# Performance work log

Hardware: AMD Instinct MI355X
Metric: run time of the kernel (lower is better)

Reference implementation:

```python
import jax, jax.numpy as jnp
import numpy as np
from jax import lax

T = 600000   # raw waveform samples (divisible by first_stride=5)
CIN = 256    # channels
L = T // 5   # output frames


def _leaky(x):
    return jnp.where(x >= 0, x, 0.3 * x)


def _quantize(x, scale, offset):
    # div + round + int8 cast + float cast; clip emulates the int8 range
    return jnp.clip(jnp.round(x / scale - offset), -128.0, 127.0)


def _dequantize(x, scale, offset):
    return (x + offset) * scale


def _conv1d(x, w, stride=1, dilation=1, groups=1):
    # x: [B, W, C]; w: [K, Cin/groups, Cout]; VALID padding (buffers provide causal pad)
    return lax.conv_general_dilated(
        x, w, window_strides=(stride,), padding='VALID',
        rhs_dilation=(dilation,), dimension_numbers=('NWC', 'WIO', 'NWC'),
        feature_group_count=groups)


def _res_block(x, w_dw, b_dw, w_pw, b_pw, w_lc, b_lc, dilation, qp=None, dqp=None):
    C = x.shape[-1]
    h = _conv1d(x, w_dw, dilation=dilation, groups=C) + b_dw   # depthwise (3,1)
    h = _conv1d(h, w_pw) + b_pw                                # pointwise 1x1
    if qp is not None:
        h = _quantize(h, *qp)
    h = _leaky(h)
    h = _conv1d(h, w_lc) + b_lc                                # last 1x1
    if dqp is not None:
        h = _dequantize(h, *dqp)
    return h


def setup_inputs() -> dict:
    key = jax.random.key(0)
    ks = jax.random.split(key, 32)
    rn = lambda k, s, sc=0.05: jax.random.normal(k, s, dtype=jnp.float32) * sc
    inp = {
        'x': rn(ks[0], (1, T, 1, 1), 1.0),
        'first_buffer': jnp.zeros((1, 5, 1, 1), jnp.float32),
        'res1_buffer': jnp.zeros((1, 2, 1, CIN), jnp.float32),
        'res2_buffer': jnp.zeros((1, 6, 1, CIN), jnp.float32),
        'res3_buffer': jnp.zeros((1, 18, 1, CIN), jnp.float32),
        'w_first': rn(ks[1], (10, 1, CIN)),
        'b_first': rn(ks[2], (CIN,)),
    }
    i = 3
    for r in (1, 2, 3):
        inp['w_dw%d' % r] = rn(ks[i], (3, 1, CIN)); i += 1
        inp['b_dw%d' % r] = rn(ks[i], (CIN,)); i += 1
        inp['w_pw%d' % r] = rn(ks[i], (1, CIN, CIN)); i += 1
        inp['b_pw%d' % r] = rn(ks[i], (CIN,)); i += 1
        inp['w_lc%d' % r] = rn(ks[i], (1, CIN, CIN)); i += 1
        inp['b_lc%d' % r] = rn(ks[i], (CIN,)); i += 1
    return inp


def reference(x, first_buffer, res1_buffer, res2_buffer, res3_buffer,
              w_first, b_first,
              w_dw1, b_dw1, w_pw1, b_pw1, w_lc1, b_lc1,
              w_dw2, b_dw2, w_pw2, b_pw2, w_lc2, b_lc2,
              w_dw3, b_dw3, w_pw3, b_pw3, w_lc3, b_lc3):
    sq = lambda a: a[:, :, 0, :]  # [B,T,1,C] -> [B,T,C]; spatial W dim is always 1
    xs = sq(jnp.concatenate([first_buffer, x], axis=1))        # causal pad: [1,T+5,1]
    res_in = _conv1d(xs, w_first, stride=5) + b_first          # [1,L,CIN]
    ci = _leaky(res_in)
    ci = jnp.concatenate([sq(res1_buffer), ci], axis=1)        # pad 2 for dil-1 k3
    ro = _res_block(ci, w_dw1, b_dw1, w_pw1, b_pw1, w_lc1, b_lc1, dilation=1,
                    qp=(17.62967872619629, -67.0), dqp=(6.528060436248779, -16.0))
    res_in = res_in + ro
    res_in = _quantize(res_in, 12.716455459594727, -23.0)
    ci = _dequantize(_leaky(res_in), 5.548006534576416, 47.0)
    ci = jnp.concatenate([sq(res2_buffer), ci], axis=1)        # pad 6 for dil-3 k3
    ci = _quantize(ci, 5.548006534576416, 47.0)
    ro = _res_block(ci, w_dw2, b_dw2, w_pw2, b_pw2, w_lc2, b_lc2, dilation=3)
    res_in = ro + res_in
    ci = _dequantize(_leaky(res_in), 4.458680152893066, 38.0)
    ci = jnp.concatenate([sq(res3_buffer), ci], axis=1)        # pad 18 for dil-9 k3
    ci = _quantize(ci, 4.458680152893066, 38.0)
    ro = _res_block(ci, w_dw3, b_dw3, w_pw3, b_pw3, w_lc3, b_lc3, dilation=9)
    res_in = ro + res_in
    out = _dequantize(_leaky(res_in), 3.698859930038452, 34.0)
    return out[:, :, None, :]  # [1, L, 1, CIN]
```

## Files before the change

### kernel.cpp

```cpp
#include <hip/hip_runtime.h>


#define CIN   256
#define LOUT  120000
#define TIN   600000
#define FB    128
#define NBLK  ((LOUT + FB - 1) / FB)

typedef float fx4 __attribute__((ext_vector_type(4)));
typedef short bx8 __attribute__((ext_vector_type(8)));

#define BF_OFF   0
#define CI1_OFF  32768
#define R2R_OFF  50176
#define C3R_OFF  60056
#define XW_OFF   73056
#define LUT_OFF  73760
#define LDS_SZ   74016

__device__ __forceinline__ float lrelu(float v){ return v >= 0.0f ? v : 0.3f*v; }
__device__ __forceinline__ float clip8(float v){ return fminf(fmaxf(v, -128.0f), 127.0f); }
__device__ __forceinline__ unsigned short f2bf(float f){
  unsigned u = __builtin_bit_cast(unsigned, f);
  return (unsigned short)((u + 0x7FFFu + ((u >> 16) & 1u)) >> 16);
}
__device__ __forceinline__ float bf2f(unsigned short h){
  unsigned u = ((unsigned)h) << 16;
  return __builtin_bit_cast(float, u);
}
__device__ __forceinline__ unsigned cvtpk(float a, float b){
  unsigned r;
  asm("v_cvt_pk_bf16_f32 %0, %1, %2" : "=v"(r) : "v"(a), "v"(b));
  return r;
}

__device__ __forceinline__ void gemm_mfma(const char* __restrict__ Aw,
                                          const char* __restrict__ Bf,
                                          int lofs, fx4 acc[2][2])
{
#pragma unroll 1
  for (int kk = 0; kk < 8; ++kk) {
    bx8 Bh0 = *(const bx8*)(Bf + kk*4096 +        lofs);
    bx8 Bl0 = *(const bx8*)(Bf + kk*4096 + 1024 + lofs);
    bx8 Bh1 = *(const bx8*)(Bf + kk*4096 + 2048 + lofs);
    bx8 Bl1 = *(const bx8*)(Bf + kk*4096 + 3072 + lofs);
#pragma unroll
    for (int mt = 0; mt < 2; ++mt) {
      bx8 Ah = *(const bx8*)(Aw + (mt*8 + kk)*2048 +        lofs);
      bx8 Al = *(const bx8*)(Aw + (mt*8 + kk)*2048 + 1024 + lofs);
      acc[mt][0] = __builtin_amdgcn_mfma_f32_16x16x32_bf16(Ah, Bh0, acc[mt][0], 0, 0, 0);
      acc[mt][0] = __builtin_amdgcn_mfma_f32_16x16x32_bf16(Al, Bh0, acc[mt][0], 0, 0, 0);
      acc[mt][0] = __builtin_amdgcn_mfma_f32_16x16x32_bf16(Ah, Bl0, acc[mt][0], 0, 0, 0);
      acc[mt][1] = __builtin_amdgcn_mfma_f32_16x16x32_bf16(Ah, Bh1, acc[mt][1], 0, 0, 0);
      acc[mt][1] = __builtin_amdgcn_mfma_f32_16x16x32_bf16(Al, Bh1, acc[mt][1], 0, 0, 0);
      acc[mt][1] = __builtin_amdgcn_mfma_f32_16x16x32_bf16(Ah, Bl1, acc[mt][1], 0, 0, 0);
    }
  }
}

__global__ void pack_w(const float* __restrict__ w0, const float* __restrict__ w1,
                       const float* __restrict__ w2, const float* __restrict__ w3,
                       const float* __restrict__ w4, const float* __restrict__ w5,
                       char* __restrict__ Apk)
{
  const int l = blockIdx.x*256 + threadIdx.x;
  const int lane = l & 63, kk = (l >> 6) & 7, wm = (l >> 9) & 15, mat = l >> 13;
  const float* W = mat==0?w0 : mat==1?w1 : mat==2?w2 : mat==3?w3 : mat==4?w4 : w5;
  const int oc = wm*16 + (lane & 15);
  const int k0 = kk*32 + (lane >> 4)*8;
  unsigned short h[8], lo[8];
#pragma unroll
  for (int j = 0; j < 8; ++j) {
    const float v = W[(k0 + j)*CIN + oc];
    h[j]  = f2bf(v);
    lo[j] = f2bf(v - bf2f(h[j]));
  }
  char* base = Apk + mat*262144 + (wm*8 + kk)*2048 + lane*16;
  *(ushort4*)(base)        = make_ushort4(h[0],  h[1],  h[2],  h[3]);
  *(ushort4*)(base + 8)    = make_ushort4(h[4],  h[5],  h[6],  h[7]);
  *(ushort4*)(base + 1024) = make_ushort4(lo[0], lo[1], lo[2], lo[3]);
  *(ushort4*)(base + 1032) = make_ushort4(lo[4], lo[5], lo[6], lo[7]);
}

__launch_bounds__(512, 4)
__global__ void enc_kernel(const float* __restrict__ x,
                           const char* __restrict__ Apk,
                           const float* __restrict__ w_first, const float* __restrict__ b_first,
                           const float* __restrict__ w_dw1, const float* __restrict__ b_dw1,
                           const float* __restrict__ b_pw1, const float* __restrict__ b_lc1,
                           const float* __restrict__ w_dw2, const float* __restrict__ b_dw2,
                           const float* __restrict__ b_pw2, const float* __restrict__ b_lc2,
                           const float* __restrict__ w_dw3, const float* __restrict__ b_dw3,
                           const float* __restrict__ b_pw3, const float* __restrict__ b_lc3,
                           float* __restrict__ out)
{
  __shared__ __align__(16) char lds[LDS_SZ];
  const int tid  = threadIdx.x;
  const int lane = tid & 63;
  const int wv   = tid >> 6;
  const int qq   = lane >> 4;
  const int nn   = lane & 15;
  const int lofs = lane * 16;
  const int ch   = tid & 255;
  const int hf   = tid >> 8;
  const int t0   = blockIdx.x * FB;
  const fx4 fz = {0.0f, 0.0f, 0.0f, 0.0f};
  const char* Awv = Apk + wv*32768;

  volatile int vz = 0;

  if (tid < 256) {
    const float r  = (float)(tid - 128);
    const float dq = (lrelu(r) + 47.0f) * 5.548006534576416f;
    const float c  = clip8(rintf(dq / 5.548006534576416f - 47.0f));
    *(signed char*)&lds[LUT_OFF + tid] = (signed char)(int)c;
  }

  const int wofs_c = (ch >> 5)*4096 + (((ch & 31) >> 3)*16)*16 + (ch & 7)*2;

  int c0m[2];
#pragma unroll
  for (int mt = 0; mt < 2; ++mt) c0m[mt] = wv*32 + mt*16 + qq*4;

  fx4 acc[2][2];

  for (int pass = 0; pass < 5; ++pass) {
    const int pt0 = t0 - 32 + pass*32;
    const int xbase = 5*pt0 - 15;

    const int z = vz;
    const float* wfq  = w_first + z; const float* bfq  = b_first + z;
    const float* wd1q = w_dw1 + z;   const float* bd1q = b_dw1 + z;
    const float* wd2q = w_dw2 + z;   const float* bd2q = b_dw2 + z;
    const float* wd3q = w_dw3 + z;   const float* bd3q = b_dw3 + z;
    const float* bp1q = b_pw1 + z;   const float* bl1q = b_lc1 + z;
    const float* bp2q = b_pw2 + z;   const float* bl2q = b_lc2 + z;
    const float* bp3q = b_pw3 + z;   const float* bl3q = b_lc3 + z;

    float resf[2][2][4];

    __syncthreads();
    if (tid < 176) {
      const int gx = xbase + tid;
      *(float*)&lds[XW_OFF + tid*4] = (gx >= 0 && gx < TIN) ? x[gx] : 0.0f;
    }
    __syncthreads();

    {
      float wf[10];
#pragma unroll
      for (int k = 0; k < 10; ++k) wf[k] = wfq[k*CIN + ch];
      const float bfv = bfq[ch];
      const int j0 = hf * 17;
      for (int j = j0; j < j0 + 17; ++j) {
        const int t = pt0 + j - 2;
        float a = 0.0f;
#pragma unroll
        for (int k = 0; k < 10; ++k)
          a = fmaf(*(const float*)&lds[XW_OFF + (5*j + k)*4], wf[k], a);
        const float ci = (t < 0) ? 0.0f : lrelu(a + bfv);
        *(unsigned short*)&lds[CI1_OFF + (ch*34 + j)*2] = (unsigned short)cvtpk(ci, ci);
      }
    }
    __syncthreads();

    {
      const float d10 = wd1q[ch], d11 = wd1q[CIN+ch], d12 = wd1q[2*CIN+ch];
      const float bd1 = bd1q[ch];
      for (int s = 0; s < 16; ++s) {
        const int jr = hf*16 + ((s + tid) & 15);
        const float c2 = bf2f(*(const unsigned short*)&lds[CI1_OFF + (ch*34 + jr    )*2]);
        const float c1 = bf2f(*(const unsigned short*)&lds[CI1_OFF + (ch*34 + jr + 1)*2]);
        const float c0 = bf2f(*(const unsigned short*)&lds[CI1_OFF + (ch*34 + jr + 2)*2]);
        const float v = fmaf(d10, c2, fmaf(d11, c1, fmaf(d12, c0, bd1)));
        const int ab = wofs_c + ((jr >> 4)*2048) + ((jr & 15)*16);
        const unsigned hp = cvtpk(v, v);
        const float hb = __builtin_bit_cast(float, hp << 16);
        const unsigned lp = cvtpk(v - hb, v - hb);
        *(unsigned short*)&lds[BF_OFF + ab]        = (unsigned short)hp;
        *(unsigned short*)&lds[BF_OFF + ab + 1024] = (unsigned short)lp;
      }
    }
    __syncthreads();

#pragma unroll
    for (int mt = 0; mt < 2; ++mt) { acc[mt][0] = fz; acc[mt][1] = fz; }
    gemm_mfma(Awv + 0*262144, (const char*)lds + BF_OFF, lofs, acc);
    __syncthreads();
#pragma unroll
    for (int mt = 0; mt < 2; ++mt) {
      const int c0 = c0m[mt];
      const float4 bb = *(const float4*)&bp1q[c0];
      const float bbv[4] = {bb.x, bb.y, bb.z, bb.w};
      const int ab0 = (c0 >> 5)*4096 + (((c0 & 31) >> 3)*16 + nn)*16 + (c0 & 7)*2;
#pragma unroll
      for (int nt = 0; nt < 2; ++nt) {
        float av[4];
#pragma unroll
        for (int r = 0; r < 4; ++r) {
          const float h  = acc[mt][nt][r] + bbv[r];
          const float qv = clip8(rintf(h / 17.62967872619629f + 67.0f));
          av[r] = lrelu(qv);
        }
        const unsigned h01 = cvtpk(av[0], av[1]);
        const unsigned h23 = cvtpk(av[2], av[3]);
        const float hb0 = __builtin_bit_cast(float, h01 << 16);
        const float hb1 = __builtin_bit_cast(float, h01 & 0xFFFF0000u);
        const float hb2 = __builtin_bit_cast(float, h23 << 16);
        const float hb3 = __builtin_bit_cast(float, h23 & 0xFFFF0000u);
        const unsigned l01 = cvtpk(av[0]-hb0, av[1]-hb1);
        const unsigned l23 = cvtpk(av[2]-hb2, av[3]-hb3);
        const int ab = ab0 + nt*2048;
        *(uint2*)&lds[BF_OFF + ab]        = make_uint2(h01, h23);
        *(uint2*)&lds[BF_OFF + ab + 1024] = make_uint2(l01, l23);
      }
    }
    __syncthreads();

#pragma unroll
    for (int mt = 0; mt < 2; ++mt) { acc[mt][0] = fz; acc[mt][1] = fz; }
    gemm_mfma(Awv + 1*262144, (const char*)lds + BF_OFF, lofs, acc);
    __syncthreads();
#pragma unroll
    for (int mt = 0; mt < 2; ++mt) {
      const int c0 = c0m[mt];
      float r10[4] = {0.0f, 0.0f, 0.0f, 0.0f};
      float r11[4] = {0.0f, 0.0f, 0.0f, 0.0f};
#pragma unroll 2
      for (int k = 0; k < 10; ++k) {
        const float4 wk = *(const float4*)&wfq[k*CIN + c0];
        const float x0 = *(const float*)&lds[XW_OFF + (5*nn        + 10 + k)*4];
        const float x1 = *(const float*)&lds[XW_OFF + (5*(16 + nn) + 10 + k)*4];
        r10[0] = fmaf(x0, wk.x, r10[0]); r10[1] = fmaf(x0, wk.y, r10[1]);
        r10[2] = fmaf(x0, wk.z, r10[2]); r10[3] = fmaf(x0, wk.w, r10[3]);
        r11[0] = fmaf(x1, wk.x, r11[0]); r11[1] = fmaf(x1, wk.y, r11[1]);
        r11[2] = fmaf(x1, wk.z, r11[2]); r11[3] = fmaf(x1, wk.w, r11[3]);
      }
      const float4 bl = *(const float4*)&bl1q[c0];
      const float4 bf = *(const float4*)&bfq[c0];
      const float blv[4] = {bl.x, bl.y, bl.z, bl.w};
      const float bfa[4] = {bf.x, bf.y, bf.z, bf.w};
      {
        const int t = pt0 + nn;
        const int slot = (t + 3800) % 38;
        int pk = 0;
#pragma unroll
        for (int r = 0; r < 4; ++r) {
          const float ro1 = (acc[mt][0][r] + blv[r] - 16.0f) * 6.528060436248779f;
          const float v   = (r10[r] + bfa[r]) + ro1;
          const float q   = clip8(rintf(v / 12.716455459594727f + 23.0f));
          pk |= ((int)q & 255) << (8*r);
        }
        *(int*)&lds[R2R_OFF + slot*260 + c0] = pk;
      }
      {
        const int t = pt0 + 16 + nn;
        const int slot = (t + 3800) % 38;
        int pk = 0;
#pragma unroll
        for (int r = 0; r < 4; ++r) {
          const float ro1 = (acc[mt][1][r] + blv[r] - 16.0f) * 6.528060436248779f;
          const float v   = (r11[r] + bfa[r]) + ro1;
          const float q   = clip8(rintf(v / 12.716455459594727f + 23.0f));
          pk |= ((int)q & 255) << (8*r);
        }
        *(int*)&lds[R2R_OFF + slot*260 + c0] = pk;
      }
    }
    __syncthreads();

    {
      const float d20 = wd2q[ch], d21 = wd2q[CIN+ch], d22 = wd2q[2*CIN+ch];
      const float bd2 = bd2q[ch];
      for (int s = 0; s < 16; ++s) {
        const int jr = hf*16 + ((s + tid) & 15);
        const int t = pt0 + jr;
        float cv[3];
#pragma unroll
        for (int li = 0; li < 3; ++li) {
          const int tt = t - 3*(2 - li);
          float c;
          if (tt < 0) c = -47.0f;
          else {
            const int sl = (tt + 3800) % 38;
            const int rv = (int)*(const signed char*)&lds[R2R_OFF + sl*260 + ch];
            c = (float)*(const signed char*)&lds[LUT_OFF + 128 + rv];
          }
          cv[li] = c;
        }
        const float v = fmaf(d20, cv[0], fmaf(d21, cv[1], fmaf(d22, cv[2], bd2)));
        const int ab = wofs_c + ((jr >> 4)*2048) + ((jr & 15)*16);
        const unsigned hp = cvtpk(v, v);
        const float hb = __builtin_bit_cast(float, hp << 16);
        const unsigned lp = cvtpk(v - hb, v - hb);
        *(unsigned short*)&lds[BF_OFF + ab]        = (unsigned short)hp;
        *(unsigned short*)&lds[BF_OFF + ab + 1024] = (unsigned short)lp;
      }
    }
    __syncthreads();

#pragma unroll
    for (int mt = 0; mt < 2; ++mt) { acc[mt][0] = fz; acc[mt][1] = fz; }
    gemm_mfma(Awv + 2*262144, (const char*)lds + BF_OFF, lofs, acc);
    __syncthreads();
#pragma unroll
    for (int mt = 0; mt < 2; ++mt) {
      const int c0 = c0m[mt];
      const float4 bb = *(const float4*)&bp2q[c0];
      const float bbv[4] = {bb.x, bb.y, bb.z, bb.w};
      const int ab0 = (c0 >> 5)*4096 + (((c0 & 31) >> 3)*16 + nn)*16 + (c0 & 7)*2;
#pragma unroll
      for (int nt = 0; nt < 2; ++nt) {
        float av[4];
#pragma unroll
        for (int r = 0; r < 4; ++r)
          av[r] = lrelu(acc[mt][nt][r] + bbv[r]);
        const unsigned h01 = cvtpk(av[0], av[1]);
        const unsigned h23 = cvtpk(av[2], av[3]);
        const float hb0 = __builtin_bit_cast(float, h01 << 16);
        const float hb1 = __builtin_bit_cast(float, h01 & 0xFFFF0000u);
        const float hb2 = __builtin_bit_cast(float, h23 << 16);
        const float hb3 = __builtin_bit_cast(float, h23 & 0xFFFF0000u);
        const unsigned l01 = cvtpk(av[0]-hb0, av[1]-hb1);
        const unsigned l23 = cvtpk(av[2]-hb2, av[3]-hb3);
        const int ab = ab0 + nt*2048;
        *(uint2*)&lds[BF_OFF + ab]        = make_uint2(h01, h23);
        *(uint2*)&lds[BF_OFF + ab + 1024] = make_uint2(l01, l23);
      }
    }
    __syncthreads();

#pragma unroll
    for (int mt = 0; mt < 2; ++mt) { acc[mt][0] = fz; acc[mt][1] = fz; }
    gemm_mfma(Awv + 3*262144, (const char*)lds + BF_OFF, lofs, acc);
    __syncthreads();
#pragma unroll
    for (int nt = 0; nt < 2; ++nt) {
      const int t = pt0 + nt*16 + nn;
      const int slot  = (t + 5000) % 50;
      const int slot2 = (t + 3800) % 38;
#pragma unroll
      for (int mt = 0; mt < 2; ++mt) {
        const int c0 = c0m[mt];
        const int pk2 = *(const int*)&lds[R2R_OFF + slot2*260 + c0];
        const float4 bl = *(const float4*)&bl2q[c0];
        const float blv[4] = {bl.x, bl.y, bl.z, bl.w};
        int pk = 0;
#pragma unroll
        for (int r = 0; r < 4; ++r) {
          const float qold = (float)((signed char)((pk2 >> (8*r)) & 255));
          const float r3 = (acc[mt][nt][r] + blv[r]) + qold;
          resf[mt][nt][r] = r3;
          const float dq = (lrelu(r3) + 38.0f) * 4.458680152893066f;
          const float q  = clip8(rintf(dq / 4.458680152893066f - 38.0f));
          pk |= ((int)q & 255) << (8*r);
        }
        *(int*)&lds[C3R_OFF + slot*260 + c0] = pk;
      }
    }
    __syncthreads();

    if (pass == 0) continue;

    {
      const float d30 = wd3q[ch], d31 = wd3q[CIN+ch], d32 = wd3q[2*CIN+ch];
      const float bd3 = bd3q[ch];
      for (int s = 0; s < 16; ++s) {
        const int jr = hf*16 + ((s + tid) & 15);
        const int t = pt0 + jr;
        float cv[3];
#pragma unroll
        for (int li = 0; li < 3; ++li) {
          const int tt = t - 9*(2 - li);
          float c;
          if (tt < 0) c = -38.0f;
          else {
            const int sl = (tt + 5000) % 50;
            c = (float)*(const signed char*)&lds[C3R_OFF + sl*260 + ch];
          }
          cv[li] = c;
        }
        const float v = fmaf(d30, cv[0], fmaf(d31, cv[1], fmaf(d32, cv[2], bd3)));
        const int ab = wofs_c + ((jr >> 4)*2048) + ((jr & 15)*16);
        const unsigned hp = cvtpk(v, v);
        const float hb = __builtin_bit_cast(float, hp << 16);
        const unsigned lp = cvtpk(v - hb, v - hb);
        *(unsigned short*)&lds[BF_OFF + ab]        = (unsigned short)hp;
        *(unsigned short*)&lds[BF_OFF + ab + 1024] = (unsigned short)lp;
      }
    }
    __syncthreads();

#pragma unroll
    for (int mt = 0; mt < 2; ++mt) { acc[mt][0] = fz; acc[mt][1] = fz; }
    gemm_mfma(Awv + 4*262144, (const char*)lds + BF_OFF, lofs, acc);
    __syncthreads();
#pragma unroll
    for (int mt = 0; mt < 2; ++mt) {
      const int c0 = c0m[mt];
      const float4 bb = *(const float4*)&bp3q[c0];
      const float bbv[4] = {bb.x, bb.y, bb.z, bb.w};
      const int ab0 = (c0 >> 5)*4096 + (((c0 & 31) >> 3)*16 + nn)*16 + (c0 & 7)*2;
#pragma unroll
      for (int nt = 0; nt < 2; ++nt) {
        float av[4];
#pragma unroll
        for (int r = 0; r < 4; ++r)
          av[r] = lrelu(acc[mt][nt][r] + bbv[r]);
        const unsigned h01 = cvtpk(av[0], av[1]);
        const unsigned h23 = cvtpk(av[2], av[3]);
        const float hb0 = __builtin_bit_cast(float, h01 << 16);
        const float hb1 = __builtin_bit_cast(float, h01 & 0xFFFF0000u);
        const float hb2 = __builtin_bit_cast(float, h23 << 16);
        const float hb3 = __builtin_bit_cast(float, h23 & 0xFFFF0000u);
        const unsigned l01 = cvtpk(av[0]-hb0, av[1]-hb1);
        const unsigned l23 = cvtpk(av[2]-hb2, av[3]-hb3);
        const int ab = ab0 + nt*2048;
        *(uint2*)&lds[BF_OFF + ab]        = make_uint2(h01, h23);
        *(uint2*)&lds[BF_OFF + ab + 1024] = make_uint2(l01, l23);
      }
    }
    __syncthreads();

#pragma unroll
    for (int mt = 0; mt < 2; ++mt) { acc[mt][0] = fz; acc[mt][1] = fz; }
    gemm_mfma(Awv + 5*262144, (const char*)lds + BF_OFF, lofs, acc);
#pragma unroll
    for (int nt = 0; nt < 2; ++nt) {
      const int t = pt0 + nt*16 + nn;
      if (t < LOUT) {
#pragma unroll
        for (int mt = 0; mt < 2; ++mt) {
          const int c0 = c0m[mt];
          const float4 bl = *(const float4*)&bl3q[c0];
          const float blv[4] = {bl.x, bl.y, bl.z, bl.w};
          fx4 o;
#pragma unroll
          for (int r = 0; r < 4; ++r) {
            const float r4 = (acc[mt][nt][r] + blv[r]) + resf[mt][nt][r];
            o[r] = (lrelu(r4) + 34.0f) * 3.698859930038452f;
          }
          __builtin_nontemporal_store(o, (fx4*)&out[t*CIN + c0]);
        }
      }
    }
  }
}

extern "C" void kernel_launch(void* const* d_in, const int* in_sizes, int n_in,
                              void* d_out, int out_size, void* d_ws, size_t ws_size,
                              hipStream_t stream) {
  (void)in_sizes; (void)n_in; (void)out_size; (void)ws_size;
  const float* x       = (const float*)d_in[0];
  const float* w_first = (const float*)d_in[5];
  const float* b_first = (const float*)d_in[6];
  const float* w_dw1   = (const float*)d_in[7];
  const float* b_dw1   = (const float*)d_in[8];
  const float* w_pw1   = (const float*)d_in[9];
  const float* b_pw1   = (const float*)d_in[10];
  const float* w_lc1   = (const float*)d_in[11];
  const float* b_lc1   = (const float*)d_in[12];
  const float* w_dw2   = (const float*)d_in[13];
  const float* b_dw2   = (const float*)d_in[14];
  const float* w_pw2   = (const float*)d_in[15];
  const float* b_pw2   = (const float*)d_in[16];
  const float* w_lc2   = (const float*)d_in[17];
  const float* b_lc2   = (const float*)d_in[18];
  const float* w_dw3   = (const float*)d_in[19];
  const float* b_dw3   = (const float*)d_in[20];
  const float* w_pw3   = (const float*)d_in[21];
  const float* b_pw3   = (const float*)d_in[22];
  const float* w_lc3   = (const float*)d_in[23];
  const float* b_lc3   = (const float*)d_in[24];

  char* Apk = (char*)d_ws;

  pack_w<<<dim3(192), dim3(256), 0, stream>>>(w_pw1, w_lc1, w_pw2, w_lc2, w_pw3, w_lc3, Apk);
  enc_kernel<<<dim3(NBLK), dim3(512), 0, stream>>>(
      x, Apk, w_first, b_first,
      w_dw1, b_dw1, b_pw1, b_lc1,
      w_dw2, b_dw2, b_pw2, b_lc2,
      w_dw3, b_dw3, b_pw3, b_lc3,
      (float*)d_out);
}
```

Baseline: 768.2 us.

## Fuse first conv into depthwise stage via registers and drop redundant barriers

The stride-5 first convolution outputs now stay in registers, with each thread computing two extra halo frames, and feed the dilation-1 depthwise conv directly. This removes the bf16 round trip through the CI1 LDS buffer and the barrier between the two stages. Three more __syncthreads are also removed: one at the start of each pass and the ones after the second and fourth GEMMs. In exchange there is a little redundant first-conv work and more register pressure, and a data race is possible if any of the removed barriers was protecting LDS reuse.

Measured after the change: 993.9 us. 29.4% more time.

```diff
diff --git a/kernel.cpp b/kernel.cpp
--- a/kernel.cpp
+++ b/kernel.cpp
@@ -103,6 +103,7 @@
   const int lofs = lane * 16;
   const int ch   = tid & 255;
   const int hf   = tid >> 8;
+  const int rot  = tid & 15;
   const int t0   = blockIdx.x * FB;
   const fx4 fz = {0.0f, 0.0f, 0.0f, 0.0f};
   const char* Awv = Apk + wv*32768;
@@ -139,7 +140,6 @@
 
     float resf[2][2][4];
 
-    __syncthreads();
     if (tid < 176) {
       const int gx = xbase + tid;
       *(float*)&lds[XW_OFF + tid*4] = (gx >= 0 && gx < TIN) ? x[gx] : 0.0f;
@@ -151,27 +151,38 @@
 #pragma unroll
       for (int k = 0; k < 10; ++k) wf[k] = wfq[k*CIN + ch];
       const float bfv = bfq[ch];
-      const int j0 = hf * 17;
-      for (int j = j0; j < j0 + 17; ++j) {
-        const int t = pt0 + j - 2;
+      float c[16], cb0, cb1;
+#pragma unroll
+      for (int u = 0; u < 16; ++u) {
+        const int j = hf*16 + ((u + rot) & 15);
         float a = 0.0f;
 #pragma unroll
         for (int k = 0; k < 10; ++k)
           a = fmaf(*(const float*)&lds[XW_OFF + (5*j + k)*4], wf[k], a);
-        const float ci = (t < 0) ? 0.0f : lrelu(a + bfv);
-        *(unsigned short*)&lds[CI1_OFF + (ch*34 + j)*2] = (unsigned short)cvtpk(ci, ci);
-      }
-    }
-    __syncthreads();
-
-    {
+        const float ci = (pt0 + j - 2 < 0) ? 0.0f : lrelu(a + bfv);
+        c[u] = __builtin_bit_cast(float, cvtpk(ci, ci) << 16);
+      }
+#pragma unroll
+      for (int b = 0; b < 2; ++b) {
+        const int j = hf*16 + 16 + b;
+        float a = 0.0f;
+#pragma unroll
+        for (int k = 0; k < 10; ++k)
+          a = fmaf(*(const float*)&lds[XW_OFF + (5*j + k)*4], wf[k], a);
+        const float ci = (pt0 + j - 2 < 0) ? 0.0f : lrelu(a + bfv);
+        const float cv = __builtin_bit_cast(float, cvtpk(ci, ci) << 16);
+        if (b == 0) cb0 = cv; else cb1 = cv;
+      }
       const float d10 = wd1q[ch], d11 = wd1q[CIN+ch], d12 = wd1q[2*CIN+ch];
       const float bd1 = bd1q[ch];
+#pragma unroll
       for (int s = 0; s < 16; ++s) {
-        const int jr = hf*16 + ((s + tid) & 15);
-        const float c2 = bf2f(*(const unsigned short*)&lds[CI1_OFF + (ch*34 + jr    )*2]);
-        const float c1 = bf2f(*(const unsigned short*)&lds[CI1_OFF + (ch*34 + jr + 1)*2]);
-        const float c0 = bf2f(*(const unsigned short*)&lds[CI1_OFF + (ch*34 + jr + 2)*2]);
+        const int jloc = (s + rot) & 15;
+        const int jr = hf*16 + jloc;
+        const float c2 = c[s];
+        const float c1 = (jloc == 15) ? cb0 : c[(s + 1) & 15];
+        const float c0 = (jloc == 15) ? cb1 :
+                         ((jloc == 14) ? cb0 : c[(s + 2) & 15]);
         const float v = fmaf(d10, c2, fmaf(d11, c1, fmaf(d12, c0, bd1)));
         const int ab = wofs_c + ((jr >> 4)*2048) + ((jr & 15)*16);
         const unsigned hp = cvtpk(v, v);
@@ -220,7 +231,6 @@
 #pragma unroll
     for (int mt = 0; mt < 2; ++mt) { acc[mt][0] = fz; acc[mt][1] = fz; }
     gemm_mfma(Awv + 1*262144, (const char*)lds + BF_OFF, lofs, acc);
-    __syncthreads();
 #pragma unroll
     for (int mt = 0; mt < 2; ++mt) {
       const int c0 = c0m[mt];
@@ -333,7 +343,6 @@
 #pragma unroll
     for (int mt = 0; mt < 2; ++mt) { acc[mt][0] = fz; acc[mt][1] = fz; }
     gemm_mfma(Awv + 3*262144, (const char*)lds + BF_OFF, lofs, acc);
-    __syncthreads();
 #pragma unroll
     for (int nt = 0; nt < 2; ++nt) {
       const int t = pt0 + nt*16 + nn;
```
